# Kernel optimization log

Hardware: AMD Instinct MI355X
Metric: run time of the kernel (lower is better)

The kernel has to match this reference:

```python
import jax, jax.numpy as jnp
import numpy as np

N_EMBD = 2048
DIM_ATT = 2048
HEAD_SIZE = 64
N_HEAD = DIM_ATT // HEAD_SIZE
N_LAYER = 24
LAYER_ID = 12
CHUNK_LEN = 512
HEAD_DIV = 8
B = 4
TT = 4096


def _init_params():
    ratio_0_to_1 = LAYER_ID / (N_LAYER - 1)
    ratio_1_to_almost0 = 1.0 - LAYER_ID / N_LAYER
    ddd = (np.arange(N_EMBD) / N_EMBD).reshape(1, 1, N_EMBD).astype(np.float32)
    time_mix_k = np.power(ddd, ratio_1_to_almost0)
    time_mix_v = np.power(ddd, ratio_1_to_almost0) + 0.3 * ratio_0_to_1
    time_mix_r = np.power(ddd, 0.5 * ratio_1_to_almost0)
    time_mix_g = np.power(ddd, 0.5 * ratio_1_to_almost0)
    h = np.arange(N_HEAD, dtype=np.float32)
    time_decay = -8 + 7 * (h / (N_HEAD - 1)) ** (0.7 + 1.3 * ratio_0_to_1)
    time_faaaa = np.full(N_HEAD, 0.05, dtype=np.float32)
    return (jnp.asarray(time_mix_k), jnp.asarray(time_mix_v), jnp.asarray(time_mix_r),
            jnp.asarray(time_mix_g), jnp.asarray(time_decay.astype(np.float32)), jnp.asarray(time_faaaa))


def setup_inputs() -> dict:
    key = jax.random.key(0)
    ks = jax.random.split(key, 8)
    scale = 1.0 / np.sqrt(N_EMBD)
    x = jax.random.normal(ks[0], (B, TT, N_EMBD), dtype=jnp.float32)
    W_r = jax.random.normal(ks[1], (N_EMBD, DIM_ATT), dtype=jnp.float32) * scale
    W_k = jax.random.normal(ks[2], (N_EMBD, DIM_ATT), dtype=jnp.float32) * scale
    W_v = jax.random.normal(ks[3], (N_EMBD, DIM_ATT), dtype=jnp.float32) * scale
    W_g = jax.random.normal(ks[4], (N_EMBD, DIM_ATT), dtype=jnp.float32) * scale
    W_o = jax.random.normal(ks[5], (DIM_ATT, N_EMBD), dtype=jnp.float32) * scale
    ln_gamma = jnp.ones((DIM_ATT,), dtype=jnp.float32)
    ln_beta = jnp.zeros((DIM_ATT,), dtype=jnp.float32)
    tmk, tmv, tmr, tmg, tdecay, tfaaaa = _init_params()
    state0 = jnp.zeros((B, N_HEAD, HEAD_SIZE, HEAD_SIZE), dtype=jnp.float32)
    return dict(x=x, W_r=W_r, W_k=W_k, W_v=W_v, W_g=W_g, W_o=W_o,
                ln_gamma=ln_gamma, ln_beta=ln_beta,
                time_mix_k=tmk, time_mix_v=tmv, time_mix_r=tmr, time_mix_g=tmg,
                time_decay=tdecay, time_faaaa=tfaaaa, state0=state0)


def _group_norm(x, gamma, beta, num_groups, eps=1e-5):
    # x: [N, C]
    N, C = x.shape
    xg = x.reshape(N, num_groups, C // num_groups)
    mean = xg.mean(axis=-1, keepdims=True)
    var = xg.var(axis=-1, keepdims=True)
    xn = (xg - mean) * jax.lax.rsqrt(var + eps)
    return xn.reshape(N, C) * gamma + beta


def _decay_mats(time_decay, time_faaaa, T):
    w1 = jnp.exp(-jnp.exp(time_decay))[:, None]              # [H,1]
    u = time_faaaa[:, None]                                  # [H,1]
    ws = (w1 ** T).reshape(1, N_HEAD, 1, 1)                  # [1,H,1,1]
    ind = jnp.arange(T - 1, -1, -1, dtype=jnp.float32)[None, :]  # [1,T]
    w = w1 ** ind                                            # [H,T] decays T-1..0
    wk = w.reshape(1, N_HEAD, 1, T)
    wb = jnp.flip(wk, axis=-1).swapaxes(-2, -1)              # [1,H,T,1]
    wcat = jnp.concatenate([w[:, 1:], u], axis=1)            # [H,T]
    wpad = jnp.pad(wcat, ((0, 0), (0, T)))                   # [H,2T]
    wt = jnp.tile(wpad, (1, T))[:, :-T].reshape(N_HEAD, T, 2 * T - 1)
    wmat = wt[:, :, T - 1:].reshape(1, N_HEAD, T, T)         # intra-chunk matrix
    return wmat, wk, wb, ws


def reference(x, W_r, W_k, W_v, W_g, W_o, ln_gamma, ln_beta,
              time_mix_k, time_mix_v, time_mix_r, time_mix_g,
              time_decay, time_faaaa, state0):
    Bx, T_total, C = x.shape
    H, S = N_HEAD, HEAD_SIZE
    T = min(CHUNK_LEN, T_total)

    # time shift: prepend zeros (initial TimeShift state)
    xx = jnp.concatenate([jnp.zeros((Bx, 1, C), x.dtype), x[:, :-1, :]], axis=1)
    xk = x * time_mix_k + xx * (1 - time_mix_k)
    xv = x * time_mix_v + xx * (1 - time_mix_v)
    xr = x * time_mix_r + xx * (1 - time_mix_r)
    xg = x * time_mix_g + xx * (1 - time_mix_g)

    r = (xr @ W_r).reshape(Bx, T_total, H, S).transpose(0, 2, 1, 3)   # [B,H,TT,S]
    k = (xk @ W_k).reshape(Bx, T_total, H, S).transpose(0, 2, 3, 1)   # [B,H,S,TT]
    v = (xv @ W_v).reshape(Bx, T_total, H, S).transpose(0, 2, 1, 3)   # [B,H,TT,S]
    g = jax.nn.silu(xg @ W_g)                                         # [B,TT,C]

    wmat, wk, wb, ws = _decay_mats(time_decay, time_faaaa, T)
    wmat = wmat.astype(r.dtype); wk = wk.astype(r.dtype)
    wb = wb.astype(r.dtype); ws = ws.astype(r.dtype)

    nchunks = T_total // T
    # reshape into chunks: [nchunks, B, H, T, S]
    rc = r.reshape(Bx, H, nchunks, T, S).transpose(2, 0, 1, 3, 4)
    kc = k.reshape(Bx, H, S, nchunks, T).transpose(3, 0, 1, 2, 4)   # [n,B,H,S,T]
    vc = v.reshape(Bx, H, nchunks, T, S).transpose(2, 0, 1, 3, 4)

    def step(s, inp):
        rr, kk, vv = inp  # [B,H,T,S], [B,H,S,T], [B,H,T,S]
        att = (rr @ kk) * wmat                  # [B,H,T,T]
        out = att @ vv + (rr @ s) * wb          # [B,H,T,S]
        s_new = ws * s + (kk * wk) @ vv         # [B,H,S,S]
        return s_new, out

    s_final, xs = jax.lax.scan(step, state0.astype(r.dtype), (rc, kc, vc))
    # xs: [n,B,H,T,S] -> [B,H,TT,S]
    xout = xs.transpose(1, 2, 0, 3, 4).reshape(Bx, H, T_total, S)
    xout = xout.transpose(0, 2, 1, 3).reshape(Bx * T_total, H * S)
    xout = _group_norm(xout / HEAD_DIV, ln_gamma, ln_beta, H)
    xout = xout.reshape(Bx, T_total, H * S) * g
    return xout @ W_o
```

## Files before the change

kernel.cpp:

```cpp
#include <hip/hip_runtime.h>

typedef unsigned short u16;
typedef short short8 __attribute__((ext_vector_type(8)));
typedef float f32x4 __attribute__((ext_vector_type(4)));

struct __attribute__((aligned(8), may_alias)) U2 { unsigned int x, y; };
struct __attribute__((aligned(16), may_alias)) U4 { unsigned int x, y, z, w; };
struct __attribute__((aligned(16), may_alias)) F4 { float x, y, z, w; };

__device__ __forceinline__ float bf2f(u16 h) {
    union { unsigned int u; float f; } x; x.u = ((unsigned int)h) << 16; return x.f;
}
__device__ __forceinline__ u16 f2bf(float f) {
    union { float f; unsigned int u; } x; x.f = f;
    return (u16)((x.u + 0x7FFFu + ((x.u >> 16) & 1u)) >> 16);
}
__device__ __forceinline__ short8 lds8(const u16* p) {
    union { U2 q[2]; short8 s; } u;
    u.q[0] = *(const U2*)p;
    u.q[1] = *(const U2*)(p + 4);
    return u.s;
}
__device__ __forceinline__ void gl_lds16(const u16* g, u16* l) {
    __builtin_amdgcn_global_load_lds(
        (const __attribute__((address_space(1))) void*)g,
        (__attribute__((address_space(3))) void*)l, 16, 0, 0);
}

__global__ void transpose5(const float* __restrict__ s0, const float* __restrict__ s1,
                           const float* __restrict__ s2, const float* __restrict__ s3,
                           const float* __restrict__ s4,
                           u16* __restrict__ d0, u16* __restrict__ d1,
                           u16* __restrict__ d2, u16* __restrict__ d3,
                           u16* __restrict__ d4)
{
    const float* S; u16* D;
    switch (blockIdx.z) {
        case 0: S = s0; D = d0; break;
        case 1: S = s1; D = d1; break;
        case 2: S = s2; D = d2; break;
        case 3: S = s3; D = d3; break;
        default: S = s4; D = d4; break;
    }
    __shared__ float tile[32][33];
    int tx = threadIdx.x, ty = threadIdx.y;
    int bx = blockIdx.x * 32, by = blockIdx.y * 32;
    #pragma unroll
    for (int i = 0; i < 32; i += 8)
        tile[ty + i][tx] = S[(size_t)(by + ty + i) * 2048 + bx + tx];
    __syncthreads();
    #pragma unroll
    for (int i = 0; i < 32; i += 8)
        D[(size_t)(bx + ty + i) * 2048 + by + tx] = f2bf(tile[tx][ty + i]);
}

__global__ __launch_bounds__(256, 4) void mix2_rows(
    const float* __restrict__ x, const float* __restrict__ tmA,
    const float* __restrict__ tmB, u16* __restrict__ outA, u16* __restrict__ outB)
{
    const int t = blockIdx.x;
    const int c = threadIdx.x * 8;
    const float* xp = x + (size_t)t * 2048 + c;
    const bool first = (t & 4095) == 0;
    F4 a0 = *(const F4*)xp, a1 = *(const F4*)(xp + 4);
    F4 p0 = {0.f, 0.f, 0.f, 0.f}, p1 = {0.f, 0.f, 0.f, 0.f};
    if (!first) { p0 = *(const F4*)(xp - 2048); p1 = *(const F4*)(xp - 2048 + 4); }
    F4 ta0 = *(const F4*)(tmA + c), ta1 = *(const F4*)(tmA + c + 4);
    F4 tb0 = *(const F4*)(tmB + c), tb1 = *(const F4*)(tmB + c + 4);
    float xc[8] = {a0.x, a0.y, a0.z, a0.w, a1.x, a1.y, a1.z, a1.w};
    float xq[8] = {p0.x, p0.y, p0.z, p0.w, p1.x, p1.y, p1.z, p1.w};
    float ma[8] = {ta0.x, ta0.y, ta0.z, ta0.w, ta1.x, ta1.y, ta1.z, ta1.w};
    float mb[8] = {tb0.x, tb0.y, tb0.z, tb0.w, tb1.x, tb1.y, tb1.z, tb1.w};
    union { u16 s[8]; U4 v; } oa, ob;
    #pragma unroll
    for (int e = 0; e < 8; ++e) {
        float d = xc[e] - xq[e];
        oa.s[e] = f2bf(xq[e] + ma[e] * d);
        ob.s[e] = f2bf(xq[e] + mb[e] * d);
    }
    *(U4*)(outA + (size_t)t * 2048 + c) = oa.v;
    *(U4*)(outB + (size_t)t * 2048 + c) = ob.v;
}

__device__ __forceinline__ void storeC(u16* p, float v) { *p = f2bf(v); }
__device__ __forceinline__ void storeC(float* p, float v) { *p = v; }

template <typename CT>
__global__ __launch_bounds__(256, 1) void gemm_bt(
    const u16* __restrict__ A, const u16* __restrict__ Bt, CT* __restrict__ C,
    int M, int N, int K)
{
    __shared__ u16 As[128][32];
    __shared__ u16 Bs[128][32];
    const int tid = threadIdx.x;
    const int lane = tid & 63, wv = tid >> 6;
    const int quad = lane >> 4, l16 = lane & 15;
    const int wm = (wv >> 1) * 64, wn = (wv & 1) * 64;
    const int bm = blockIdx.x * 128, bn = blockIdx.y * 128;

    const int sr = tid >> 2, ss = tid & 3;
    const u16* ga0 = A + (size_t)(bm + sr) * K + ss * 8;
    const u16* ga1 = A + (size_t)(bm + sr + 64) * K + ss * 8;
    const u16* gb0 = Bt + (size_t)(bn + sr) * K + ss * 8;
    const u16* gb1 = Bt + (size_t)(bn + sr + 64) * K + ss * 8;
    u16* la0 = &As[sr][ss * 8];
    u16* la1 = &As[sr + 64][ss * 8];
    u16* lb0 = &Bs[sr][ss * 8];
    u16* lb1 = &Bs[sr + 64][ss * 8];

    f32x4 acc[4][4];
    const f32x4 zero4 = {0.f, 0.f, 0.f, 0.f};
    #pragma unroll
    for (int i = 0; i < 4; ++i)
        #pragma unroll
        for (int j = 0; j < 4; ++j) acc[i][j] = zero4;

    for (int k0 = 0; k0 < K; k0 += 32) {
        __syncthreads();
        gl_lds16(ga0 + k0, la0);
        gl_lds16(ga1 + k0, la1);
        gl_lds16(gb0 + k0, lb0);
        gl_lds16(gb1 + k0, lb1);
        __syncthreads();
        short8 af[4], bfv[4];
        #pragma unroll
        for (int mt = 0; mt < 4; ++mt) af[mt] = lds8(&As[wm + mt * 16 + l16][quad * 8]);
        #pragma unroll
        for (int nt = 0; nt < 4; ++nt) bfv[nt] = lds8(&Bs[wn + nt * 16 + l16][quad * 8]);
        #pragma unroll
        for (int mt = 0; mt < 4; ++mt)
            #pragma unroll
            for (int nt = 0; nt < 4; ++nt)
                acc[mt][nt] = __builtin_amdgcn_mfma_f32_16x16x32_bf16(
                    af[mt], bfv[nt], acc[mt][nt], 0, 0, 0);
    }
    #pragma unroll
    for (int mt = 0; mt < 4; ++mt)
        #pragma unroll
        for (int nt = 0; nt < 4; ++nt)
            #pragma unroll
            for (int r = 0; r < 4; ++r) {
                int row = bm + wm + mt * 16 + quad * 4 + r;
                int col = bn + wn + nt * 16 + l16;
                storeC(&C[(size_t)row * N + col], acc[mt][nt][r]);
            }
}

__global__ __launch_bounds__(256, 2) void wkv_state(
    const u16* __restrict__ Kb, const u16* __restrict__ Vb,
    const float* __restrict__ td, float* __restrict__ Sc)
{
    __shared__ u16 ktT[64][72];
    __shared__ u16 vtT[64][72];
    __shared__ float wpow[512];

    const int blk = blockIdx.x;
    const int c = blk & 7, h = (blk >> 3) & 31, b = blk >> 8;
    const int tid = threadIdx.x;
    const int w = tid >> 6, lane = tid & 63;
    const int quad = lane >> 4, l16 = lane & 15;

    const float E = expf(td[h]);
    for (int p = tid; p < 512; p += 256) wpow[p] = expf(-(float)p * E);

    const size_t rowbase = ((size_t)b * 4096 + c * 512) * 2048 + (size_t)h * 64;
    const f32x4 zero4 = {0.f, 0.f, 0.f, 0.f};
    f32x4 acc[4];
    #pragma unroll
    for (int nt = 0; nt < 4; ++nt) acc[nt] = zero4;
    __syncthreads();

    for (int J = 0; J < 8; ++J) {
        __syncthreads();
        #pragma unroll
        for (int it = 0; it < 2; ++it) {
            int slot = it * 256 + tid;
            int row = slot >> 3, seg = slot & 7;
            size_t goff = rowbase + (size_t)(J * 64 + row) * 2048 + seg * 8;
            union { U4 v; u16 s[8]; } kv, vv;
            kv.v = *(const U4*)(Kb + goff);
            vv.v = *(const U4*)(Vb + goff);
            float wp = wpow[511 - (J * 64 + row)];
            #pragma unroll
            for (int e = 0; e < 8; ++e) {
                ktT[seg * 8 + e][row] = f2bf(bf2f(kv.s[e]) * wp);
                vtT[seg * 8 + e][row] = vv.s[e];
            }
        }
        __syncthreads();
        short8 a0 = lds8(&ktT[w * 16 + l16][quad * 8]);
        short8 a1 = lds8(&ktT[w * 16 + l16][32 + quad * 8]);
        #pragma unroll
        for (int nt = 0; nt < 4; ++nt) {
            short8 b0 = lds8(&vtT[nt * 16 + l16][quad * 8]);
            short8 b1 = lds8(&vtT[nt * 16 + l16][32 + quad * 8]);
            acc[nt] = __builtin_amdgcn_mfma_f32_16x16x32_bf16(a0, b0, acc[nt], 0, 0, 0);
            acc[nt] = __builtin_amdgcn_mfma_f32_16x16x32_bf16(a1, b1, acc[nt], 0, 0, 0);
        }
    }
    float* out = Sc + ((size_t)((b * 32 + h) * 8 + c) << 12);
    #pragma unroll
    for (int nt = 0; nt < 4; ++nt)
        #pragma unroll
        for (int r = 0; r < 4; ++r)
            out[(w * 16 + quad * 4 + r) * 64 + nt * 16 + l16] = acc[nt][r];
}

__global__ __launch_bounds__(256, 4) void wkv_scan(
    const float* __restrict__ Sc, const float* __restrict__ st0,
    const float* __restrict__ td, u16* __restrict__ SinT)
{
    const int blk = blockIdx.x;
    const int h = blk & 31;
    const int tid = threadIdx.x;
    const int s2 = tid & 63;
    const int s1b = (tid >> 6) * 16;
    const float wsT = expf(-512.f * expf(td[h]));

    float S[16];
    const float* sp = st0 + ((size_t)blk << 12);
    #pragma unroll
    for (int i = 0; i < 16; ++i) S[i] = sp[(s1b + i) * 64 + s2];

    const size_t base = ((size_t)blk * 8) << 12;
    for (int c = 0; c < 8; ++c) {
        u16* op = SinT + base + ((size_t)c << 12) + s2 * 64 + s1b;
        union { u16 s[16]; U4 v[2]; } ov;
        #pragma unroll
        for (int i = 0; i < 16; ++i) ov.s[i] = f2bf(S[i]);
        *(U4*)op = ov.v[0];
        *(U4*)(op + 8) = ov.v[1];
        if (c < 7) {
            const float* cp = Sc + base + ((size_t)c << 12);
            #pragma unroll
            for (int i = 0; i < 16; ++i)
                S[i] = wsT * S[i] + cp[(s1b + i) * 64 + s2];
        }
    }
}

__global__ __launch_bounds__(512, 1) void wkv_out(
    const u16* __restrict__ Rb, const u16* __restrict__ Kb,
    const u16* __restrict__ Vb, const u16* __restrict__ Gb,
    const u16* __restrict__ SinT,
    const float* __restrict__ td, const float* __restrict__ tf,
    const float* __restrict__ gamma, const float* __restrict__ beta,
    u16* __restrict__ Xout)
{
    __shared__ u16 kt[64][72];
    __shared__ u16 vtT[64][72];
    __shared__ u16 Pb[8][64][40];
    __shared__ float wpow[513];

    const int blk = blockIdx.x;
    const int c = blk & 7, h = (blk >> 3) & 31, b = blk >> 8;
    const int tid = threadIdx.x;
    const int w = tid >> 6, lane = tid & 63;
    const int quad = lane >> 4, l16 = lane & 15;

    const float E = expf(td[h]);
    const float u = tf[h];
    for (int p = tid; p <= 512; p += 512) wpow[p] = expf(-(float)p * E);

    const size_t rowbase = ((size_t)b * 4096 + c * 512) * 2048 + (size_t)h * 64;
    const f32x4 zero4 = {0.f, 0.f, 0.f, 0.f};
    __syncthreads();

    short8 ar[4][2];
    #pragma unroll
    for (int mt = 0; mt < 4; ++mt)
        #pragma unroll
        for (int ks = 0; ks < 2; ++ks) {
            int t = w * 64 + mt * 16 + l16;
            const u16* p = Rb + rowbase + (size_t)t * 2048 + ks * 32 + quad * 8;
            union { U4 v; short8 s; } uu; uu.v = *(const U4*)p;
            ar[mt][ks] = uu.s;
        }

    const u16* sp = SinT + ((size_t)((b * 32 + h) * 8 + c) << 12);
    f32x4 acc[4][4];
    #pragma unroll
    for (int i = 0; i < 4; ++i)
        #pragma unroll
        for (int j = 0; j < 4; ++j) acc[i][j] = zero4;
    #pragma unroll
    for (int ks = 0; ks < 2; ++ks)
        #pragma unroll
        for (int nt = 0; nt < 4; ++nt) {
            union { U4 v; short8 s; } uu;
            uu.v = *(const U4*)(sp + (nt * 16 + l16) * 64 + ks * 32 + quad * 8);
            short8 bs = uu.s;
            #pragma unroll
            for (int mt = 0; mt < 4; ++mt)
                acc[mt][nt] = __builtin_amdgcn_mfma_f32_16x16x32_bf16(
                    ar[mt][ks], bs, acc[mt][nt], 0, 0, 0);
        }
    #pragma unroll
    for (int mt = 0; mt < 4; ++mt)
        #pragma unroll
        for (int r = 0; r < 4; ++r) {
            float f = wpow[w * 64 + mt * 16 + quad * 4 + r];
            #pragma unroll
            for (int nt = 0; nt < 4; ++nt) acc[mt][nt][r] *= f;
        }

    for (int J = 0; J < 8; ++J) {
        __syncthreads();
        {
            int row = tid >> 3, seg = tid & 7;
            size_t goff = rowbase + (size_t)(J * 64 + row) * 2048 + seg * 8;
            union { U4 v; u16 s[8]; } kv, vv;
            kv.v = *(const U4*)(Kb + goff);
            vv.v = *(const U4*)(Vb + goff);
            *(U4*)&kt[row][seg * 8] = kv.v;
            #pragma unroll
            for (int e = 0; e < 8; ++e) vtT[seg * 8 + e][row] = vv.s[e];
        }
        __syncthreads();
        if (w >= J) {
            #pragma unroll
            for (int half = 0; half < 2; ++half) {
                #pragma unroll
                for (int jt2 = 0; jt2 < 2; ++jt2) {
                    int jt = half * 2 + jt2;
                    short8 bk0 = lds8(&kt[jt * 16 + l16][quad * 8]);
                    short8 bk1 = lds8(&kt[jt * 16 + l16][32 + quad * 8]);
                    #pragma unroll
                    for (int mt = 0; mt < 4; ++mt) {
                        f32x4 s4 = zero4;
                        s4 = __builtin_amdgcn_mfma_f32_16x16x32_bf16(ar[mt][0], bk0, s4, 0, 0, 0);
                        s4 = __builtin_amdgcn_mfma_f32_16x16x32_bf16(ar[mt][1], bk1, s4, 0, 0, 0);
                        int ibase = w * 64 + mt * 16 + quad * 4;
                        int j = J * 64 + jt * 16 + l16;
                        #pragma unroll
                        for (int r = 0; r < 4; ++r) {
                            int i = ibase + r;
                            float f = (j < i) ? wpow[i - j - 1] : ((j == i) ? u : 0.f);
                            Pb[w][mt * 16 + quad * 4 + r][jt2 * 16 + l16] = f2bf(s4[r] * f);
                        }
                    }
                }
                __builtin_amdgcn_wave_barrier();
                short8 ap[4];
                #pragma unroll
                for (int mt = 0; mt < 4; ++mt)
                    ap[mt] = lds8(&Pb[w][mt * 16 + l16][quad * 8]);
                #pragma unroll
                for (int nt = 0; nt < 4; ++nt) {
                    short8 bv = lds8(&vtT[nt * 16 + l16][half * 32 + quad * 8]);
                    #pragma unroll
                    for (int mt = 0; mt < 4; ++mt)
                        acc[mt][nt] = __builtin_amdgcn_mfma_f32_16x16x32_bf16(
                            ap[mt], bv, acc[mt][nt], 0, 0, 0);
                }
            }
        }
    }

    #pragma unroll
    for (int mt = 0; mt < 4; ++mt) {
        float rsum[4], rsq[4];
        #pragma unroll
        for (int r = 0; r < 4; ++r) {
            float s = 0.f, sq = 0.f;
            #pragma unroll
            for (int nt = 0; nt < 4; ++nt) {
                float v = acc[mt][nt][r];
                s += v; sq += v * v;
            }
            rsum[r] = s; rsq[r] = sq;
        }
        #pragma unroll
        for (int off = 1; off < 16; off <<= 1)
            #pragma unroll
            for (int r = 0; r < 4; ++r) {
                rsum[r] += __shfl_xor(rsum[r], off);
                rsq[r] += __shfl_xor(rsq[r], off);
            }
        #pragma unroll
        for (int r = 0; r < 4; ++r) {
            float mean = rsum[r] * (1.f / 512.f);
            float var = rsq[r] * (1.f / 4096.f) - mean * mean;
            float rstd = rsqrtf(var + 1e-5f);
            int tg = w * 64 + mt * 16 + quad * 4 + r;
            size_t obase = rowbase + (size_t)tg * 2048;
            #pragma unroll
            for (int nt = 0; nt < 4; ++nt) {
                int ch = nt * 16 + l16;
                float y = acc[mt][nt][r] * 0.125f;
                float xn = (y - mean) * rstd * gamma[h * 64 + ch] + beta[h * 64 + ch];
                float gl = bf2f(Gb[obase + ch]);
                float sg = gl / (1.f + expf(-gl));
                Xout[obase + ch] = f2bf(xn * sg);
            }
        }
    }
}

extern "C" void kernel_launch(void* const* d_in, const int* in_sizes, int n_in,
                              void* d_out, int out_size, void* d_ws, size_t ws_size,
                              hipStream_t stream)
{
    const float* x   = (const float*)d_in[0];
    const float* Wr  = (const float*)d_in[1];
    const float* Wk  = (const float*)d_in[2];
    const float* Wv  = (const float*)d_in[3];
    const float* Wg  = (const float*)d_in[4];
    const float* Wo  = (const float*)d_in[5];
    const float* gam = (const float*)d_in[6];
    const float* bet = (const float*)d_in[7];
    const float* tmk = (const float*)d_in[8];
    const float* tmv = (const float*)d_in[9];
    const float* tmr = (const float*)d_in[10];
    const float* tmg = (const float*)d_in[11];
    const float* td  = (const float*)d_in[12];
    const float* tf  = (const float*)d_in[13];
    const float* st0 = (const float*)d_in[14];
    float* out = (float*)d_out;

    char* ws = (char*)d_ws;
    const size_t WSZ = (size_t)2048 * 2048 * 2;
    const size_t ASZ = (size_t)16384 * 2048 * 2;
    u16* WtR = (u16*)(ws + 0 * WSZ);
    u16* WtK = (u16*)(ws + 1 * WSZ);
    u16* WtV = (u16*)(ws + 2 * WSZ);
    u16* WtG = (u16*)(ws + 3 * WSZ);
    u16* WtO = (u16*)(ws + 4 * WSZ);
    char* act = ws + 5 * WSZ;
    u16* rb = (u16*)(act + 0 * ASZ);
    u16* kb = (u16*)(act + 1 * ASZ);
    u16* vb = (u16*)(act + 2 * ASZ);
    u16* gb = (u16*)(act + 3 * ASZ);
    u16* xo = gb;

    u16* mixA = (u16*)d_out;
    u16* mixB = (u16*)d_out + (size_t)16384 * 2048;
    float* ScBuf = (float*)d_out;
    u16* SinT = (u16*)((char*)d_out + (size_t)1024 * 4096 * 4);

    transpose5<<<dim3(64, 64, 5), dim3(32, 8), 0, stream>>>(
        Wr, Wk, Wv, Wg, Wo, WtR, WtK, WtV, WtG, WtO);

    dim3 ggrid(128, 16), gblk(256);
    dim3 mgrid(16384), mblk(256);

    mix2_rows<<<mgrid, mblk, 0, stream>>>(x, tmr, tmk, mixA, mixB);
    gemm_bt<u16><<<ggrid, gblk, 0, stream>>>(mixA, WtR, rb, 16384, 2048, 2048);
    gemm_bt<u16><<<ggrid, gblk, 0, stream>>>(mixB, WtK, kb, 16384, 2048, 2048);
    mix2_rows<<<mgrid, mblk, 0, stream>>>(x, tmv, tmg, mixA, mixB);
    gemm_bt<u16><<<ggrid, gblk, 0, stream>>>(mixA, WtV, vb, 16384, 2048, 2048);
    gemm_bt<u16><<<ggrid, gblk, 0, stream>>>(mixB, WtG, gb, 16384, 2048, 2048);

    wkv_state<<<dim3(1024), dim3(256), 0, stream>>>(kb, vb, td, ScBuf);
    wkv_scan<<<dim3(128), dim3(256), 0, stream>>>(ScBuf, st0, td, SinT);
    wkv_out<<<dim3(1024), dim3(512), 0, stream>>>(
        rb, kb, vb, gb, SinT, td, tf, gam, bet, xo);

    gemm_bt<float><<<ggrid, gblk, 0, stream>>>(xo, WtO, out, 16384, 2048, 2048);
}
```

Before: 1.608 ms.

## Double-buffer GEMM LDS tiles, remap blocks across XCDs, factor off-diagonal decay

The GEMM now keeps two LDS buffers and issues the next K-slice's global-to-LDS loads before computing on the current one, which removes one barrier per iteration and is meant to overlap load latency with MFMA work. The GEMM grid becomes 1D with a tile remap that interleaves by 8, so neighbouring tiles land on the same XCD for L2 reuse. In wkv_out, off-diagonal chunk blocks compute the decay factor as a product of a per-row and a per-column power, replacing the per-element branch and gather. The factorised decay depends on wpow being an exact geometric sequence and may differ slightly in rounding. The extra LDS buffer doubles GEMM shared memory.

```diff
diff --git a/kernel.cpp b/kernel.cpp
--- a/kernel.cpp
+++ b/kernel.cpp
@@ -90,23 +90,23 @@
     const u16* __restrict__ A, const u16* __restrict__ Bt, CT* __restrict__ C,
     int M, int N, int K)
 {
-    __shared__ u16 As[128][32];
-    __shared__ u16 Bs[128][32];
+    __shared__ u16 As[2][128][32];
+    __shared__ u16 Bs[2][128][32];
     const int tid = threadIdx.x;
     const int lane = tid & 63, wv = tid >> 6;
     const int quad = lane >> 4, l16 = lane & 15;
     const int wm = (wv >> 1) * 64, wn = (wv & 1) * 64;
-    const int bm = blockIdx.x * 128, bn = blockIdx.y * 128;
+
+    const int wgid = blockIdx.x;
+    const int tile = (wgid & 7) * 256 + (wgid >> 3);
+    const int bm = (tile >> 4) * 128;
+    const int bn = (tile & 15) * 128;
 
     const int sr = tid >> 2, ss = tid & 3;
     const u16* ga0 = A + (size_t)(bm + sr) * K + ss * 8;
     const u16* ga1 = A + (size_t)(bm + sr + 64) * K + ss * 8;
     const u16* gb0 = Bt + (size_t)(bn + sr) * K + ss * 8;
     const u16* gb1 = Bt + (size_t)(bn + sr + 64) * K + ss * 8;
-    u16* la0 = &As[sr][ss * 8];
-    u16* la1 = &As[sr + 64][ss * 8];
-    u16* lb0 = &Bs[sr][ss * 8];
-    u16* lb1 = &Bs[sr + 64][ss * 8];
 
     f32x4 acc[4][4];
     const f32x4 zero4 = {0.f, 0.f, 0.f, 0.f};
@@ -115,24 +115,34 @@
         #pragma unroll
         for (int j = 0; j < 4; ++j) acc[i][j] = zero4;
 
+    gl_lds16(ga0, &As[0][sr][ss * 8]);
+    gl_lds16(ga1, &As[0][sr + 64][ss * 8]);
+    gl_lds16(gb0, &Bs[0][sr][ss * 8]);
+    gl_lds16(gb1, &Bs[0][sr + 64][ss * 8]);
+    __syncthreads();
+
+    int cur = 0;
     for (int k0 = 0; k0 < K; k0 += 32) {
-        __syncthreads();
-        gl_lds16(ga0 + k0, la0);
-        gl_lds16(ga1 + k0, la1);
-        gl_lds16(gb0 + k0, lb0);
-        gl_lds16(gb1 + k0, lb1);
-        __syncthreads();
+        if (k0 + 32 < K) {
+            int nxt = cur ^ 1;
+            gl_lds16(ga0 + k0 + 32, &As[nxt][sr][ss * 8]);
+            gl_lds16(ga1 + k0 + 32, &As[nxt][sr + 64][ss * 8]);
+            gl_lds16(gb0 + k0 + 32, &Bs[nxt][sr][ss * 8]);
+            gl_lds16(gb1 + k0 + 32, &Bs[nxt][sr + 64][ss * 8]);
+        }
         short8 af[4], bfv[4];
         #pragma unroll
-        for (int mt = 0; mt < 4; ++mt) af[mt] = lds8(&As[wm + mt * 16 + l16][quad * 8]);
-        #pragma unroll
-        for (int nt = 0; nt < 4; ++nt) bfv[nt] = lds8(&Bs[wn + nt * 16 + l16][quad * 8]);
+        for (int mt = 0; mt < 4; ++mt) af[mt] = lds8(&As[cur][wm + mt * 16 + l16][quad * 8]);
+        #pragma unroll
+        for (int nt = 0; nt < 4; ++nt) bfv[nt] = lds8(&Bs[cur][wn + nt * 16 + l16][quad * 8]);
         #pragma unroll
         for (int mt = 0; mt < 4; ++mt)
             #pragma unroll
             for (int nt = 0; nt < 4; ++nt)
                 acc[mt][nt] = __builtin_amdgcn_mfma_f32_16x16x32_bf16(
                     af[mt], bfv[nt], acc[mt][nt], 0, 0, 0);
+        __syncthreads();
+        cur ^= 1;
     }
     #pragma unroll
     for (int mt = 0; mt < 4; ++mt)
@@ -303,6 +313,13 @@
             #pragma unroll
             for (int nt = 0; nt < 4; ++nt) acc[mt][nt][r] *= f;
         }
+
+    float wAr[4][4];
+    #pragma unroll
+    for (int mt = 0; mt < 4; ++mt)
+        #pragma unroll
+        for (int r = 0; r < 4; ++r)
+            wAr[mt][r] = wpow[mt * 16 + quad * 4 + r];
 
     for (int J = 0; J < 8; ++J) {
         __syncthreads();
@@ -325,18 +342,32 @@
                     int jt = half * 2 + jt2;
                     short8 bk0 = lds8(&kt[jt * 16 + l16][quad * 8]);
                     short8 bk1 = lds8(&kt[jt * 16 + l16][32 + quad * 8]);
-                    #pragma unroll
-                    for (int mt = 0; mt < 4; ++mt) {
-                        f32x4 s4 = zero4;
-                        s4 = __builtin_amdgcn_mfma_f32_16x16x32_bf16(ar[mt][0], bk0, s4, 0, 0, 0);
-                        s4 = __builtin_amdgcn_mfma_f32_16x16x32_bf16(ar[mt][1], bk1, s4, 0, 0, 0);
-                        int ibase = w * 64 + mt * 16 + quad * 4;
-                        int j = J * 64 + jt * 16 + l16;
+                    if (w > J) {
+                        float wB = wpow[((w - J) << 6) - jt * 16 - l16 - 1];
                         #pragma unroll
-                        for (int r = 0; r < 4; ++r) {
-                            int i = ibase + r;
-                            float f = (j < i) ? wpow[i - j - 1] : ((j == i) ? u : 0.f);
-                            Pb[w][mt * 16 + quad * 4 + r][jt2 * 16 + l16] = f2bf(s4[r] * f);
+                        for (int mt = 0; mt < 4; ++mt) {
+                            f32x4 s4 = zero4;
+                            s4 = __builtin_amdgcn_mfma_f32_16x16x32_bf16(ar[mt][0], bk0, s4, 0, 0, 0);
+                            s4 = __builtin_amdgcn_mfma_f32_16x16x32_bf16(ar[mt][1], bk1, s4, 0, 0, 0);
+                            #pragma unroll
+                            for (int r = 0; r < 4; ++r)
+                                Pb[w][mt * 16 + quad * 4 + r][jt2 * 16 + l16] =
+                                    f2bf(s4[r] * (wAr[mt][r] * wB));
+                        }
+                    } else {
+                        #pragma unroll
+                        for (int mt = 0; mt < 4; ++mt) {
+                            f32x4 s4 = zero4;
+                            s4 = __builtin_amdgcn_mfma_f32_16x16x32_bf16(ar[mt][0], bk0, s4, 0, 0, 0);
+                            s4 = __builtin_amdgcn_mfma_f32_16x16x32_bf16(ar[mt][1], bk1, s4, 0, 0, 0);
+                            int ibase = w * 64 + mt * 16 + quad * 4;
+                            int j = J * 64 + jt * 16 + l16;
+                            #pragma unroll
+                            for (int r = 0; r < 4; ++r) {
+                                int i = ibase + r;
+                                float f = (j < i) ? wpow[i - j - 1] : ((j == i) ? u : 0.f);
+                                Pb[w][mt * 16 + quad * 4 + r][jt2 * 16 + l16] = f2bf(s4[r] * f);
+                            }
                         }
                     }
                 }
@@ -441,7 +472,7 @@
     transpose5<<<dim3(64, 64, 5), dim3(32, 8), 0, stream>>>(
         Wr, Wk, Wv, Wg, Wo, WtR, WtK, WtV, WtG, WtO);
 
-    dim3 ggrid(128, 16), gblk(256);
+    dim3 ggrid(2048), gblk(256);
     dim3 mgrid(16384), mblk(256);
 
     mix2_rows<<<mgrid, mblk, 0, stream>>>(x, tmr, tmk, mixA, mixB);
```

Measured after the change: 1.505 ms. 1.07x faster.
